# Kernel optimization log

Hardware: AMD Instinct MI355X
Metric: run time of the kernel (lower is better)

The kernel has to match this reference:

```python
import jax, jax.numpy as jnp
import numpy as np

FEATURES = 1024
DEPTH = int(np.floor(np.log2(FEATURES)))  # 10
NODES = 2 ** DEPTH - 1                    # 1023


def _unit_rows(key, shape):
    w = jax.random.normal(key, shape, dtype=jnp.float32)
    return w / jnp.linalg.norm(w, axis=-1, keepdims=True)


def setup_inputs() -> dict:
    key = jax.random.key(0)
    k_x, k_X, k_Y = jax.random.split(key, 3)
    oldx = jax.random.normal(k_x, (8, 4096, FEATURES), dtype=jnp.float32)
    X = _unit_rows(k_X, (NODES, FEATURES))  # hyperspherical-shell init
    Y = _unit_rows(k_Y, (NODES, FEATURES))
    return {"oldx": oldx, "X": X, "Y": Y}


def reference(oldx, X, Y):
    features = X.shape[-1]
    x = oldx.reshape(-1, features)            # [B, F]
    B = x.shape[0]
    cur = jnp.zeros((B,), dtype=jnp.int32)    # per-sample tree node
    y = jnp.zeros_like(x)
    for _ in range(DEPTH):                    # fixed small depth loop (10)
        Xc = X[cur]                           # [B, F] data-dependent gather
        lam = jnp.einsum('bi,bi->b', x, Xc)   # [B]
        y = y + lam[:, None] * Y[cur]         # [B, F]
        cur = cur * 2 + 1 + (lam > 0).astype(jnp.int32)
    return y.reshape(oldx.shape)
```

## Files before the change

### kernel.cpp

```cpp
#include <hip/hip_runtime.h>

#define FEAT 1024
#define DEPTH 10
#define NLEAF 1024
#define NODES (NLEAF - 1)
#define CAP 320
#define TAU 0.02f

typedef float f32x4 __attribute__((ext_vector_type(4)));

template <int CTRL, int RMASK>
__device__ __forceinline__ float dpp_shift_f(float v) {
    union { float f; int i; } u, r;
    u.f = v;
    r.i = __builtin_amdgcn_update_dpp(0, u.i, CTRL, RMASK, 0xF, true);
    return r.f;
}

__device__ __forceinline__ float wave_sum_f32(float v) {
    v += dpp_shift_f<0x111, 0xF>(v);
    v += dpp_shift_f<0x112, 0xF>(v);
    v += dpp_shift_f<0x114, 0xF>(v);
    v += dpp_shift_f<0x118, 0xF>(v);
    v += dpp_shift_f<0x142, 0xA>(v);
    v += dpp_shift_f<0x143, 0xC>(v);
    union { float f; int i; } u, r;
    u.f = v;
    r.i = __builtin_amdgcn_readlane(u.i, 63);
    return r.f;
}

template <int CTRL, int RMASK>
__device__ __forceinline__ double dpp_shift_d(double v) {
    union { double d; int i[2]; } u, r;
    u.d = v;
    r.i[0] = __builtin_amdgcn_update_dpp(0, u.i[0], CTRL, RMASK, 0xF, true);
    r.i[1] = __builtin_amdgcn_update_dpp(0, u.i[1], CTRL, RMASK, 0xF, true);
    return r.d;
}

__device__ __forceinline__ double wave_sum_f64(double v) {
    v += dpp_shift_d<0x111, 0xF>(v);
    v += dpp_shift_d<0x112, 0xF>(v);
    v += dpp_shift_d<0x114, 0xF>(v);
    v += dpp_shift_d<0x118, 0xF>(v);
    v += dpp_shift_d<0x142, 0xA>(v);
    v += dpp_shift_d<0x143, 0xC>(v);
    union { double d; int i[2]; } u, r;
    u.d = v;
    r.i[0] = __builtin_amdgcn_readlane(u.i[0], 63);
    r.i[1] = __builtin_amdgcn_readlane(u.i[1], 63);
    return r.d;
}

__device__ __forceinline__ double dot_f64_row(
    const f32x4 (&xv)[4], const float* __restrict__ Xr, int lane)
{
    double p0 = 0.0, p1 = 0.0, p2 = 0.0, p3 = 0.0;
#pragma unroll
    for (int k = 0; k < 4; ++k) {
        f32x4 xc = *reinterpret_cast<const f32x4*>(Xr + (lane + 64 * k) * 4);
        p0 += (double)xv[k][0] * (double)xc[0];
        p1 += (double)xv[k][1] * (double)xc[1];
        p2 += (double)xv[k][2] * (double)xc[2];
        p3 += (double)xv[k][3] * (double)xc[3];
    }
    return wave_sum_f64((p0 + p1) + (p2 + p3));
}

__global__ __launch_bounds__(256) void prep_kernel(
    const float* __restrict__ Xw,
    unsigned short* __restrict__ Xb,
    int* __restrict__ cursor)
{
    const int gid = blockIdx.x * 256 + threadIdx.x;
    const int r = gid >> 10;
    const int o = gid & 1023;
    const int lane = o >> 4, j = o & 15;
    const int src = ((lane + 64 * (j >> 2)) << 2) + (j & 3);

    union { float f; unsigned int u; } v;
    v.f = Xw[(size_t)r * FEAT + src];
    unsigned int u = v.u;
    u += 0x7FFFu + ((u >> 16) & 1u);
    Xb[(size_t)r * FEAT + o] = (unsigned short)(u >> 16);

    if (gid < NLEAF) cursor[gid] = 0;
}

__global__ __launch_bounds__(256) void path_kernel(
    const float* __restrict__ x,
    const float* __restrict__ Xw,
    const unsigned short* __restrict__ Xb,
    float* __restrict__ lam_out,
    int* __restrict__ order,
    int* __restrict__ cursor,
    int nsamples)
{
    const int wave = threadIdx.x >> 6;
    const int lane = threadIdx.x & 63;
    const int s0 = (blockIdx.x * 4 + wave) * 4;
    if (s0 >= nsamples) return;

    f32x4 xv[4][4];
#pragma unroll
    for (int s = 0; s < 4; ++s) {
        const float* xp = x + (size_t)(s0 + s) * FEAT;
#pragma unroll
        for (int k = 0; k < 4; ++k)
            xv[s][k] = __builtin_nontemporal_load(
                reinterpret_cast<const f32x4*>(xp + (lane + 64 * k) * 4));
    }

    int cur[4] = {0, 0, 0, 0};

#pragma unroll
    for (int d = 0; d < DEPTH; ++d) {
        uint4 q0[4], q1[4];
#pragma unroll
        for (int s = 0; s < 4; ++s) {
            const uint4* br = reinterpret_cast<const uint4*>(
                Xb + (size_t)cur[s] * FEAT + lane * 16);
            q0[s] = br[0];
            q1[s] = br[1];
        }

        float psum[4];
#pragma unroll
        for (int s = 0; s < 4; ++s) {
            const unsigned int u8[8] = {q0[s].x, q0[s].y, q0[s].z, q0[s].w,
                                        q1[s].x, q1[s].y, q1[s].z, q1[s].w};
            float a0 = 0.f, a1 = 0.f, a2 = 0.f, a3 = 0.f;
#pragma unroll
            for (int k = 0; k < 4; ++k) {
                union { unsigned int u; float f; } c0, c1, c2, c3;
                c0.u = u8[2 * k] << 16;
                c1.u = u8[2 * k] & 0xFFFF0000u;
                c2.u = u8[2 * k + 1] << 16;
                c3.u = u8[2 * k + 1] & 0xFFFF0000u;
                a0 = fmaf(xv[s][k][0], c0.f, a0);
                a1 = fmaf(xv[s][k][1], c1.f, a1);
                a2 = fmaf(xv[s][k][2], c2.f, a2);
                a3 = fmaf(xv[s][k][3], c3.f, a3);
            }
            psum[s] = wave_sum_f32((a0 + a1) + (a2 + a3));
        }

#pragma unroll
        for (int s = 0; s < 4; ++s) {
            double p;
            if (__builtin_expect(__builtin_fabsf(psum[s]) < TAU, 0))
                p = dot_f64_row(xv[s], Xw + (size_t)cur[s] * FEAT, lane);
            else
                p = (double)psum[s];
            if (lane == 0)
                lam_out[(size_t)(s0 + s) * DEPTH + d] = (float)p;
            cur[s] = 2 * cur[s] + 1 + (p > 0.0 ? 1 : 0);
        }
    }

    if (lane == 0) {
#pragma unroll
        for (int s = 0; s < 4; ++s) {
            const int b = cur[s] - NODES;
            const int pos = atomicAdd(&cursor[b], 1);
            if (pos < CAP) order[b * CAP + pos] = s0 + s;
        }
    }
}

__global__ __launch_bounds__(512) void emit_kernel(
    const float* __restrict__ Yw,
    const float* __restrict__ lam,
    const int* __restrict__ order,
    const int* __restrict__ cursor,
    float* __restrict__ out)
{
    __shared__ float ylds[DEPTH][FEAT];
    const int b = blockIdx.x >> 1;
    const int half = blockIdx.x & 1;
    const int leafPlus = b + NLEAF;

    for (int i = threadIdx.x; i < DEPTH * (FEAT / 4); i += 512) {
        const int d = i >> 8;
        const int c = i & 255;
        const int node = (leafPlus >> (DEPTH - d)) - 1;
        reinterpret_cast<f32x4*>(ylds[d])[c] =
            reinterpret_cast<const f32x4*>(Yw + (size_t)node * FEAT)[c];
    }
    __syncthreads();

    int cnt = cursor[b];
    if (cnt > CAP) cnt = CAP;
    const int wave = threadIdx.x >> 6;
    const int lane = threadIdx.x & 63;

    for (int i = half * 8 + wave; i < cnt; i += 16) {
        const int s = __builtin_amdgcn_readfirstlane(order[b * CAP + i]);

        const float* lp = lam + (size_t)s * DEPTH;
        float lm[DEPTH];
#pragma unroll
        for (int d = 0; d < DEPTH; ++d)
            lm[d] = lp[d];

        float* op = out + (size_t)s * FEAT;
#pragma unroll
        for (int k = 0; k < 4; ++k) {
            f32x4 o = (f32x4)(0.f);
#pragma unroll
            for (int d = 0; d < DEPTH; ++d)
                o += lm[d] * reinterpret_cast<const f32x4*>(ylds[d])[lane + 64 * k];
            __builtin_nontemporal_store(o, reinterpret_cast<f32x4*>(op + 4 * (lane + 64 * k)));
        }
    }
}

__global__ __launch_bounds__(256) void fff_fallback(
    const float* __restrict__ x, const float* __restrict__ Xw,
    const float* __restrict__ Yw, float* __restrict__ out, int nsamples)
{
    const int wave = threadIdx.x >> 6, lane = threadIdx.x & 63;
    const int s = blockIdx.x * 4 + wave;
    if (s >= nsamples) return;
    const float* xp = x + (size_t)s * FEAT;
    f32x4 xv[4], acc[4];
#pragma unroll
    for (int k = 0; k < 4; ++k) {
        xv[k] = *reinterpret_cast<const f32x4*>(xp + (lane + 64 * k) * 4);
        acc[k] = (f32x4)(0.f);
    }
    int cur = 0;
#pragma unroll
    for (int d = 0; d < DEPTH; ++d) {
        const float* Xr = Xw + (size_t)cur * FEAT;
        double p = 0.0;
#pragma unroll
        for (int k = 0; k < 4; ++k) {
            f32x4 xc = *reinterpret_cast<const f32x4*>(Xr + (lane + 64 * k) * 4);
            p += (double)xv[k][0] * (double)xc[0];
            p += (double)xv[k][1] * (double)xc[1];
            p += (double)xv[k][2] * (double)xc[2];
            p += (double)xv[k][3] * (double)xc[3];
        }
#pragma unroll
        for (int off = 32; off >= 1; off >>= 1) p += __shfl_xor(p, off, 64);
        const float lamv = (float)p;
        const float* Yr = Yw + (size_t)cur * FEAT;
#pragma unroll
        for (int k = 0; k < 4; ++k) {
            f32x4 yc = *reinterpret_cast<const f32x4*>(Yr + (lane + 64 * k) * 4);
            acc[k] += lamv * yc;
        }
        cur = 2 * cur + 1 + (p > 0.0 ? 1 : 0);
    }
    float* op = out + (size_t)s * FEAT;
#pragma unroll
    for (int k = 0; k < 4; ++k)
        *reinterpret_cast<f32x4*>(op + 4 * (lane + 64 * k)) = acc[k];
}

extern "C" void kernel_launch(void* const* d_in, const int* in_sizes, int n_in,
                              void* d_out, int out_size, void* d_ws, size_t ws_size,
                              hipStream_t stream) {
    const float* oldx = (const float*)d_in[0];
    const float* Xw   = (const float*)d_in[1];
    const float* Yw   = (const float*)d_in[2];
    float* out = (float*)d_out;

    const int ns = in_sizes[0] / FEAT;

    const size_t XbB   = (size_t)NODES * FEAT * sizeof(unsigned short);
    const size_t lamB  = (size_t)ns * DEPTH * sizeof(float);
    const size_t ordB  = (size_t)NLEAF * CAP * sizeof(int);
    const size_t curB  = NLEAF * sizeof(int);
    const size_t need  = XbB + lamB + ordB + curB;

    if (ws_size < need) {
        fff_fallback<<<(ns + 3) / 4, 256, 0, stream>>>(oldx, Xw, Yw, out, ns);
        return;
    }

    char* w = (char*)d_ws;
    unsigned short* Xb = (unsigned short*)w;  w += XbB;
    float* lam    = (float*)w;  w += lamB;
    int*   order  = (int*)w;    w += ordB;
    int*   cursor = (int*)w;

    prep_kernel<<<(NODES * FEAT) / 256, 256, 0, stream>>>(Xw, Xb, cursor);
    path_kernel<<<(ns + 15) / 16, 256, 0, stream>>>(oldx, Xw, Xb, lam, order, cursor, ns);
    emit_kernel<<<2 * NLEAF, 512, 0, stream>>>(Yw, lam, order, cursor, out);
}
```

Before: 109.4 us.

## Prefetch both child rows per level, one sample per wave in path kernel

The path kernel now gives each wave a single sample instead of four, and at every level speculatively loads both child node rows before the current dot product finishes. This takes the dependent gather latency off the critical path. It also rounds x to bf16 for the fast dot and reloads x from global memory in the f64 escape path, with the escape threshold widened to compensate. The cost is twice the node-row traffic, four times as many waves, and more frequent f64 fallbacks.

```diff
diff --git a/kernel.cpp b/kernel.cpp
--- a/kernel.cpp
+++ b/kernel.cpp
@@ -5,7 +5,7 @@
 #define NLEAF 1024
 #define NODES (NLEAF - 1)
 #define CAP 320
-#define TAU 0.02f
+#define TAU 0.03f
 
 typedef float f32x4 __attribute__((ext_vector_type(4)));
 
@@ -53,19 +53,28 @@
     return r.d;
 }
 
-__device__ __forceinline__ double dot_f64_row(
-    const f32x4 (&xv)[4], const float* __restrict__ Xr, int lane)
+__device__ __forceinline__ double dot_f64_escape(
+    const float* __restrict__ xp, const float* __restrict__ Xr, int lane)
 {
     double p0 = 0.0, p1 = 0.0, p2 = 0.0, p3 = 0.0;
 #pragma unroll
     for (int k = 0; k < 4; ++k) {
+        f32x4 xl = *reinterpret_cast<const f32x4*>(xp + (lane + 64 * k) * 4);
         f32x4 xc = *reinterpret_cast<const f32x4*>(Xr + (lane + 64 * k) * 4);
-        p0 += (double)xv[k][0] * (double)xc[0];
-        p1 += (double)xv[k][1] * (double)xc[1];
-        p2 += (double)xv[k][2] * (double)xc[2];
-        p3 += (double)xv[k][3] * (double)xc[3];
+        p0 += (double)xl[0] * (double)xc[0];
+        p1 += (double)xl[1] * (double)xc[1];
+        p2 += (double)xl[2] * (double)xc[2];
+        p3 += (double)xl[3] * (double)xc[3];
     }
     return wave_sum_f64((p0 + p1) + (p2 + p3));
+}
+
+__device__ __forceinline__ float bf16rnd(float f) {
+    union { float f; unsigned int u; } v;
+    v.f = f;
+    unsigned int u = v.u + (0x7FFFu + ((v.u >> 16) & 1u));
+    v.u = u & 0xFFFF0000u;
+    return v.f;
 }
 
 __global__ __launch_bounds__(256) void prep_kernel(
@@ -99,73 +108,83 @@
 {
     const int wave = threadIdx.x >> 6;
     const int lane = threadIdx.x & 63;
-    const int s0 = (blockIdx.x * 4 + wave) * 4;
-    if (s0 >= nsamples) return;
-
-    f32x4 xv[4][4];
-#pragma unroll
-    for (int s = 0; s < 4; ++s) {
-        const float* xp = x + (size_t)(s0 + s) * FEAT;
-#pragma unroll
-        for (int k = 0; k < 4; ++k)
-            xv[s][k] = __builtin_nontemporal_load(
-                reinterpret_cast<const f32x4*>(xp + (lane + 64 * k) * 4));
-    }
-
-    int cur[4] = {0, 0, 0, 0};
-
+    const int s = blockIdx.x * 4 + wave;
+    if (s >= nsamples) return;
+
+    const float* xp = x + (size_t)s * FEAT;
+
+    f32x4 xvb[4];
+#pragma unroll
+    for (int k = 0; k < 4; ++k) {
+        f32x4 t = __builtin_nontemporal_load(
+            reinterpret_cast<const f32x4*>(xp + (lane + 64 * k) * 4));
+        xvb[k][0] = bf16rnd(t[0]);
+        xvb[k][1] = bf16rnd(t[1]);
+        xvb[k][2] = bf16rnd(t[2]);
+        xvb[k][3] = bf16rnd(t[3]);
+    }
+
+    uint4 r0, r1;
+    {
+        const uint4* br = reinterpret_cast<const uint4*>(Xb + (size_t)lane * 16);
+        r0 = br[0];
+        r1 = br[1];
+    }
+
+    int cur = 0;
 #pragma unroll
     for (int d = 0; d < DEPTH; ++d) {
-        uint4 q0[4], q1[4];
-#pragma unroll
-        for (int s = 0; s < 4; ++s) {
+        uint4 cl0, cl1, cr0, cr1;
+        if (d < DEPTH - 1) {
+            const uint4* bl = reinterpret_cast<const uint4*>(
+                Xb + (size_t)(2 * cur + 1) * FEAT + lane * 16);
             const uint4* br = reinterpret_cast<const uint4*>(
-                Xb + (size_t)cur[s] * FEAT + lane * 16);
-            q0[s] = br[0];
-            q1[s] = br[1];
-        }
-
-        float psum[4];
-#pragma unroll
-        for (int s = 0; s < 4; ++s) {
-            const unsigned int u8[8] = {q0[s].x, q0[s].y, q0[s].z, q0[s].w,
-                                        q1[s].x, q1[s].y, q1[s].z, q1[s].w};
-            float a0 = 0.f, a1 = 0.f, a2 = 0.f, a3 = 0.f;
-#pragma unroll
-            for (int k = 0; k < 4; ++k) {
-                union { unsigned int u; float f; } c0, c1, c2, c3;
-                c0.u = u8[2 * k] << 16;
-                c1.u = u8[2 * k] & 0xFFFF0000u;
-                c2.u = u8[2 * k + 1] << 16;
-                c3.u = u8[2 * k + 1] & 0xFFFF0000u;
-                a0 = fmaf(xv[s][k][0], c0.f, a0);
-                a1 = fmaf(xv[s][k][1], c1.f, a1);
-                a2 = fmaf(xv[s][k][2], c2.f, a2);
-                a3 = fmaf(xv[s][k][3], c3.f, a3);
-            }
-            psum[s] = wave_sum_f32((a0 + a1) + (a2 + a3));
-        }
-
-#pragma unroll
-        for (int s = 0; s < 4; ++s) {
-            double p;
-            if (__builtin_expect(__builtin_fabsf(psum[s]) < TAU, 0))
-                p = dot_f64_row(xv[s], Xw + (size_t)cur[s] * FEAT, lane);
-            else
-                p = (double)psum[s];
-            if (lane == 0)
-                lam_out[(size_t)(s0 + s) * DEPTH + d] = (float)p;
-            cur[s] = 2 * cur[s] + 1 + (p > 0.0 ? 1 : 0);
+                Xb + (size_t)(2 * cur + 2) * FEAT + lane * 16);
+            cl0 = bl[0]; cl1 = bl[1];
+            cr0 = br[0]; cr1 = br[1];
+        }
+
+        const unsigned int u8[8] = {r0.x, r0.y, r0.z, r0.w, r1.x, r1.y, r1.z, r1.w};
+        float a0 = 0.f, a1 = 0.f, a2 = 0.f, a3 = 0.f;
+#pragma unroll
+        for (int k = 0; k < 4; ++k) {
+            union { unsigned int u; float f; } c0, c1, c2, c3;
+            c0.u = u8[2 * k] << 16;
+            c1.u = u8[2 * k] & 0xFFFF0000u;
+            c2.u = u8[2 * k + 1] << 16;
+            c3.u = u8[2 * k + 1] & 0xFFFF0000u;
+            a0 = fmaf(xvb[k][0], c0.f, a0);
+            a1 = fmaf(xvb[k][1], c1.f, a1);
+            a2 = fmaf(xvb[k][2], c2.f, a2);
+            a3 = fmaf(xvb[k][3], c3.f, a3);
+        }
+        const float p32 = wave_sum_f32((a0 + a1) + (a2 + a3));
+
+        double p;
+        if (__builtin_expect(__builtin_fabsf(p32) < TAU, 0))
+            p = dot_f64_escape(xp, Xw + (size_t)cur * FEAT, lane);
+        else
+            p = (double)p32;
+
+        if (lane == 0) lam_out[(size_t)s * DEPTH + d] = (float)p;
+        const bool right = (p > 0.0);
+        cur = 2 * cur + 1 + (right ? 1 : 0);
+
+        if (d < DEPTH - 1) {
+            asm volatile("" ::
+                "v"(cl0.x), "v"(cl0.y), "v"(cl0.z), "v"(cl0.w),
+                "v"(cl1.x), "v"(cl1.y), "v"(cl1.z), "v"(cl1.w),
+                "v"(cr0.x), "v"(cr0.y), "v"(cr0.z), "v"(cr0.w),
+                "v"(cr1.x), "v"(cr1.y), "v"(cr1.z), "v"(cr1.w));
+            r0 = right ? cr0 : cl0;
+            r1 = right ? cr1 : cl1;
         }
     }
 
     if (lane == 0) {
-#pragma unroll
-        for (int s = 0; s < 4; ++s) {
-            const int b = cur[s] - NODES;
-            const int pos = atomicAdd(&cursor[b], 1);
-            if (pos < CAP) order[b * CAP + pos] = s0 + s;
-        }
+        const int b = cur - NODES;
+        const int pos = atomicAdd(&cursor[b], 1);
+        if (pos < CAP) order[b * CAP + pos] = s;
     }
 }
 
@@ -288,6 +307,6 @@
     int*   cursor = (int*)w;
 
     prep_kernel<<<(NODES * FEAT) / 256, 256, 0, stream>>>(Xw, Xb, cursor);
-    path_kernel<<<(ns + 15) / 16, 256, 0, stream>>>(oldx, Xw, Xb, lam, order, cursor, ns);
+    path_kernel<<<(ns + 3) / 4, 256, 0, stream>>>(oldx, Xw, Xb, lam, order, cursor, ns);
     emit_kernel<<<2 * NLEAF, 512, 0, stream>>>(Yw, lam, order, cursor, out);
 }
```

Result: slower. 118.7 us (+8.5%).
